# Performance work log

Hardware: AMD Instinct MI355X
Metric: run time of the kernel (lower is better)

The kernel has to match this reference:

```python
import jax, jax.numpy as jnp
import numpy as np

N = 50000      # entities
R = 400        # relations
D = 300        # init/hidden/output dim (hard-coded 300 in module)
E = 800000     # edges over N+R nodes
B = 2048       # aligned train pairs
L = 32         # padded neighbor sequence length
H, DK = 8, 32  # n_head=8, d_k=d_v=32
GAMMA1, GAMMA2 = 0.9, 0.2


def setup_inputs() -> dict:
    key = jax.random.key(0)
    ks = iter(jax.random.split(key, 48))
    nk = lambda: next(ks)
    inp = {}
    inp["e_x"] = jax.random.normal(nk(), (N, D), jnp.float32)
    inp["r_x"] = jax.random.normal(nk(), (R, 2 * D), jnp.float32)
    inp["edge_w"] = jax.random.uniform(nk(), (E,), jnp.float32)
    # learned params (fan-in scaled)
    s = lambda fi: 1.0 / np.sqrt(fi)
    inp["Wrel"] = jax.random.normal(nk(), (2 * D, D), jnp.float32) * s(2 * D)
    inp["brel"] = jnp.zeros((D,), jnp.float32)
    inp["W1"] = jax.random.normal(nk(), (D, D), jnp.float32) * s(D)
    inp["b1"] = jnp.zeros((D,), jnp.float32)
    inp["W2"] = jax.random.normal(nk(), (D, D), jnp.float32) * s(D)
    inp["b2"] = jnp.zeros((D,), jnp.float32)
    inp["Wprox"] = jax.random.normal(nk(), (2 * D, D), jnp.float32) * s(2 * D)
    inp["bprox"] = jnp.zeros((D,), jnp.float32)
    # encoder params, index 0 = input_encoder, 1 = output_encoder
    inp["enc_Wq"] = jax.random.normal(nk(), (2, D, H * DK), jnp.float32) * s(D)
    inp["enc_Wk"] = jax.random.normal(nk(), (2, D, H * DK), jnp.float32) * s(D)
    inp["enc_Wv"] = jax.random.normal(nk(), (2, D, H * DK), jnp.float32) * s(D)
    inp["enc_Wo"] = jax.random.normal(nk(), (2, H * DK, D), jnp.float32) * s(H * DK)
    # graph structure
    inp["edge_src"] = jax.random.randint(nk(), (E,), 0, N + R, jnp.int32)
    inp["edge_dst"] = jax.random.randint(nk(), (E,), 0, N + R, jnp.int32)
    # aligned entity pairs + padded neighbor (relation, head) sequences
    inp["l_ids"] = jax.random.randint(nk(), (B,), 0, N, jnp.int32)
    inp["r_ids"] = jax.random.randint(nk(), (B,), 0, N, jnp.int32)
    for p in ("l_in", "l_out", "r_in", "r_out"):
        inp[p + "_rel"] = jax.random.randint(nk(), (B, L), 0, R, jnp.int32)
        inp[p + "_head"] = jax.random.randint(nk(), (B, L), 0, N, jnp.int32)
        inp[p + "_mask"] = jax.random.randint(nk(), (B, L), 0, 2, jnp.int32).astype(bool)
    inp["train_len"] = B
    return inp


def _cosine(x, y):
    xn = x / jnp.maximum(jnp.linalg.norm(x, axis=1, keepdims=True), 1e-8)
    yn = y / jnp.maximum(jnp.linalg.norm(y, axis=1, keepdims=True), 1e-8)
    return xn @ yn.T


def _encoder(rel_seq, head_seq, mask, kernel, ent_f, rel_f, Wq, Wk, Wv, Wo):
    # neighbor tokens: relation emb + head entity emb    [B, L, D]
    tok = ent_f[head_seq] + rel_f[rel_seq]
    b = tok.shape[0]
    q = (kernel @ Wq).reshape(b, H, DK)                  # kernel entity is the query
    k = (tok @ Wk).reshape(b, L, H, DK)
    v = (tok @ Wv).reshape(b, L, H, DK)
    scores = jnp.einsum('bhd,blhd->bhl', q, k) / np.sqrt(DK)
    scores = jnp.where(mask[:, None, :], scores, -1e9)
    attn = jax.nn.softmax(scores, axis=-1)
    ctx = jnp.einsum('bhl,blhd->bhd', attn, v).reshape(b, H * DK)
    out = ctx @ Wo                                       # [B, D]
    # entities with empty neighbor list -> zero vector (original code path)
    return jnp.where(mask.any(-1)[:, None], out, 0.0)


def _get_proximity(ids, in_rel, in_head, in_mask, out_rel, out_head, out_mask,
                   ent_f, rel_f, enc_Wq, enc_Wk, enc_Wv, enc_Wo, Wprox, bprox):
    kernel = ent_f[ids]                                  # [B, D]
    in_em = _encoder(in_rel, in_head, in_mask, kernel, ent_f, rel_f,
                     enc_Wq[0], enc_Wk[0], enc_Wv[0], enc_Wo[0])
    out_em = _encoder(out_rel, out_head, out_mask, kernel, ent_f, rel_f,
                      enc_Wq[1], enc_Wk[1], enc_Wv[1], enc_Wo[1])
    prox = jnp.concatenate([in_em, out_em], axis=1) @ Wprox + bprox
    return jnp.concatenate([kernel, prox], axis=1)       # [B, 2D]


def reference(e_x, r_x, edge_w, Wrel, brel, W1, b1, W2, b2, Wprox, bprox,
              enc_Wq, enc_Wk, enc_Wv, enc_Wo,
              edge_src, edge_dst, l_ids, r_ids,
              l_in_rel, l_in_head, l_in_mask, l_out_rel, l_out_head, l_out_mask,
              r_in_rel, r_in_head, r_in_mask, r_out_rel, r_out_head, r_out_mask,
              train_len):
    NT = N + R
    # relation_linear then relational GCN over joint entity+relation graph
    r0 = r_x @ Wrel + brel                               # [R, D]
    x = jnp.concatenate([e_x, r0], axis=0)               # [NT, D]
    agg1 = jax.ops.segment_sum(edge_w[:, None] * x[edge_src], edge_dst, num_segments=NT)
    h1 = jax.nn.relu(agg1 @ W1 + b1)
    agg2 = jax.ops.segment_sum(edge_w[:, None] * h1[edge_src], edge_dst, num_segments=NT)
    h2 = agg2 @ W2 + b2
    gcn_ex, gcn_rx = h2[:N], h2[N:]
    # proximity embeddings for left/right aligned entities
    lem = _get_proximity(l_ids, l_in_rel, l_in_head, l_in_mask,
                         l_out_rel, l_out_head, l_out_mask,
                         gcn_ex, gcn_rx, enc_Wq, enc_Wk, enc_Wv, enc_Wo, Wprox, bprox)
    rem = _get_proximity(r_ids, r_in_rel, r_in_head, r_in_mask,
                         r_out_rel, r_out_head, r_out_mask,
                         gcn_ex, gcn_rx, enc_Wq, enc_Wk, enc_Wv, enc_Wo, Wprox, bprox)
    # contrastive alignment loss
    sim = _cosine(lem, rem)                              # [B, B]
    diag = jnp.diagonal(sim)
    pos_part = jnp.mean(jnp.minimum(diag, GAMMA1))
    no_diag = sim - jnp.diag(diag)
    neg_part = jnp.mean(jnp.maximum(no_diag, GAMMA2))
    loss = neg_part - GAMMA2 - pos_part + GAMMA1
    return loss, lem, rem
```

## Files before the change

### kernel.cpp

```cpp
#include <hip/hip_runtime.h>
#include <cstdint>
#include <cstddef>

typedef _Float16 f16;
typedef __attribute__((ext_vector_type(8))) _Float16 half8;
typedef __attribute__((ext_vector_type(4))) _Float16 half4;
typedef __attribute__((ext_vector_type(4))) float f32x4;

#define NE 50000
#define NR 400
#define DD 300
#define NTOT 50400
#define EE 800000
#define BB 2048
#define LL 32
#define HD 256
#define KP1 320
#define KP2 608

__device__ inline void split2h(float x, f16& hi, f16& lo) {
  f16 h = (f16)x;
  hi = h;
  lo = (f16)(x - (float)h);
}

__global__ void convert_f16_kernel(const float4* __restrict__ src, half4* __restrict__ dst,
                                   int n4) {
  int i = blockIdx.x * blockDim.x + threadIdx.x;
  if (i < n4) {
    float4 v = src[i];
    dst[i] = (half4){(f16)v.x, (f16)v.y, (f16)v.z, (f16)v.w};
  }
}

__global__ void rel_proj_kernel(const float* __restrict__ r_x, const float* __restrict__ Wrel,
                                const float* __restrict__ brel, f16* __restrict__ out) {
  int row = blockIdx.x;
  int c = threadIdx.x;
  if (c >= DD) return;
  float acc = brel[c];
  const float* rr = r_x + (size_t)row * (2 * DD);
  for (int k = 0; k < 2 * DD; ++k) acc += rr[k] * Wrel[(size_t)k * DD + c];
  out[(size_t)row * DD + c] = (f16)acc;
}

__global__ void hist_kernel(const int* __restrict__ dst, int* __restrict__ counts) {
  int e = blockIdx.x * blockDim.x + threadIdx.x;
  if (e < EE) atomicAdd(&counts[dst[e]], 1);
}

__global__ __launch_bounds__(1024) void scan_kernel(const int* __restrict__ counts,
                                                    int* __restrict__ row_ptr,
                                                    int* __restrict__ cursor) {
  __shared__ int sums[1024];
  const int n = NTOT;
  int t = threadIdx.x;
  const int chunk = (n + 1023) / 1024;
  int begin = t * chunk;
  int end = begin + chunk; if (end > n) end = n;
  int s = 0;
  for (int i = begin; i < end; ++i) s += counts[i];
  sums[t] = s;
  __syncthreads();
  for (int off = 1; off < 1024; off <<= 1) {
    int v = (t >= off) ? sums[t - off] : 0;
    __syncthreads();
    sums[t] += v;
    __syncthreads();
  }
  int run = sums[t] - s;
  for (int i = begin; i < end; ++i) {
    row_ptr[i] = run; cursor[i] = run;
    run += counts[i];
  }
  if (t == 1023) row_ptr[n] = sums[1023];
}

__global__ void scatter_kernel(const int* __restrict__ dst, const int* __restrict__ src,
                               const float* __restrict__ w, int* __restrict__ cursor,
                               int* __restrict__ src_s, float* __restrict__ w_s) {
  int e = blockIdx.x * blockDim.x + threadIdx.x;
  if (e < EE) {
    int pos = atomicAdd(&cursor[dst[e]], 1);
    src_s[pos] = src[e];
    w_s[pos] = w[e];
  }
}

__global__ void detect_mask_kernel(const unsigned* __restrict__ m0, const unsigned* __restrict__ m1,
                                   const unsigned* __restrict__ m2, const unsigned* __restrict__ m3,
                                   int* __restrict__ flag) {
  int idx = blockIdx.x * blockDim.x + threadIdx.x;
  const int wp = BB * LL / 4;
  if (idx >= 4 * wp) return;
  const unsigned* p = idx < wp ? m0 : idx < 2 * wp ? m1 : idx < 3 * wp ? m2 : m3;
  if (p[idx % wp] > 1u) atomicOr(flag, 1);
}

__global__ void norm_mask4_kernel(const void* __restrict__ r0, const void* __restrict__ r1,
                                  const void* __restrict__ r2, const void* __restrict__ r3,
                                  int* __restrict__ outm, int* __restrict__ many,
                                  const int* __restrict__ flag) {
  int idx = blockIdx.x * blockDim.x + threadIdx.x;
  if (idx >= 4 * BB * LL) return;
  int mi = idx / (BB * LL), k = idx % (BB * LL);
  const void* raw = mi == 0 ? r0 : mi == 1 ? r1 : mi == 2 ? r2 : r3;
  int v = (*flag) ? (int)((const unsigned char*)raw)[k] : ((const int*)raw)[k];
  v = v ? 1 : 0;
  outm[idx] = v;
  if (v) atomicOr(&many[idx >> 5], 1);
}

__global__ void concat_ids_kernel(const int* __restrict__ a, const int* __restrict__ b,
                                  int* __restrict__ o) {
  int i = blockIdx.x * blockDim.x + threadIdx.x;
  if (i < BB) o[i] = a[i];
  else if (i < 2 * BB) o[i] = b[i - BB];
}

__global__ __launch_bounds__(320) void aggregate_kernel(
    const f16* __restrict__ feat, f16* __restrict__ outhi, f16* __restrict__ outlo,
    const int* __restrict__ row_ptr, const int* __restrict__ srcs, const float* __restrict__ ws) {
  int d = blockIdx.x;
  int f = threadIdx.x;
  if (f >= DD) return;
  int beg = row_ptr[d], end = row_ptr[d + 1];
  float acc = 0.f;
  int e = beg;
  for (; e + 8 <= end; e += 8) {
    int s[8]; float wv[8]; float v[8];
#pragma unroll
    for (int u = 0; u < 8; ++u) { s[u] = srcs[e + u]; wv[u] = ws[e + u]; }
#pragma unroll
    for (int u = 0; u < 8; ++u) v[u] = (float)feat[(size_t)s[u] * DD + f];
#pragma unroll
    for (int u = 0; u < 8; ++u) acc += wv[u] * v[u];
  }
  for (; e + 2 <= end; e += 2) {
    int s0 = srcs[e], s1 = srcs[e + 1];
    float w0 = ws[e], w1 = ws[e + 1];
    acc += w0 * (float)feat[(size_t)s0 * DD + f] + w1 * (float)feat[(size_t)s1 * DD + f];
  }
  if (e < end) acc += ws[e] * (float)feat[(size_t)srcs[e] * DD + f];
  f16 hi, lo; split2h(acc, hi, lo);
  outhi[(size_t)d * KP1 + f] = hi;
  outlo[(size_t)d * KP1 + f] = lo;
}

__global__ void pad_zero_kernel(f16* __restrict__ hi, f16* __restrict__ lo, int rows, int ld, int c0) {
  int pw = ld - c0;
  int idx = blockIdx.x * blockDim.x + threadIdx.x;
  if (idx >= rows * pw) return;
  int r = idx / pw, c = c0 + idx % pw;
  hi[(size_t)r * ld + c] = (f16)0.f;
  if (lo) lo[(size_t)r * ld + c] = (f16)0.f;
}

#define N_TD 11
struct TDesc {
  const float* in; f16* oh; f16* ol;
  int Kreal, Nn, Kpad, tiles_x, tile_base;
};
struct TPack { TDesc d[N_TD]; };

__global__ __launch_bounds__(256) void transpose_multi_kernel(TPack p) {
  __shared__ float tile[32][33];
  int t = blockIdx.x;
  int e = 0;
#pragma unroll
  for (int i = 1; i < N_TD; ++i)
    if (t >= p.d[i].tile_base) e = i;
  TDesc dd = p.d[e];
  int local = t - dd.tile_base;
  int k0 = (local % dd.tiles_x) * 32, n0 = (local / dd.tiles_x) * 32;
  int tx = threadIdx.x & 31, ty = threadIdx.x >> 5;
#pragma unroll
  for (int r = 0; r < 4; ++r) {
    int k = k0 + ty + r * 8, n = n0 + tx;
    float v = (k < dd.Kreal && n < dd.Nn) ? dd.in[(size_t)k * dd.Nn + n] : 0.f;
    tile[ty + r * 8][tx] = v;
  }
  __syncthreads();
#pragma unroll
  for (int r = 0; r < 4; ++r) {
    int n = n0 + ty + r * 8, k = k0 + tx;
    if (n < dd.Nn && k < dd.Kpad) {
      f16 h, l; split2h(tile[tx][ty + r * 8], h, l);
      dd.oh[(size_t)n * dd.Kpad + k] = h;
      dd.ol[(size_t)n * dd.Kpad + k] = l;
    }
  }
}

__global__ __launch_bounds__(256, 2) void mfma_gemm_kernel(
    const f16* __restrict__ Ahi, const f16* __restrict__ Alo, int lda,
    const f16* __restrict__ Bhi, const f16* __restrict__ Blo, int ldb,
    int M, int Nn, int K, const int* __restrict__ g1,
    float* __restrict__ C, int ldc, int coloff,
    const float* __restrict__ bias, int dorelu, const int* __restrict__ rowmask,
    f16* __restrict__ Chi, f16* __restrict__ Clo, int ldc16,
    int npass, int wofuse, int losfuse, double* __restrict__ accum) {
  __shared__ int4 sAh[512], sAl[512], sBh[512], sBl[512];
  const int tid = threadIdx.x;
  const int row0 = blockIdx.y * 128, col0 = blockIdx.x * 128;
  const int wave = tid >> 6, lane = tid & 63;
  const int wrow = (wave >> 1) * 64, wcol = (wave & 1) * 64;
  const int m16 = lane & 15, quad = lane >> 4;

  const int sr = tid >> 2, sc = tid & 3;
  const f16* pah[2]; const f16* pal[2]; bool va[2];
  const f16* pbh[2]; const f16* pbl[2]; bool vb[2];
  int sidx[2];
#pragma unroll
  for (int i = 0; i < 2; ++i) {
    int r = sr + i * 64;
    sidx[i] = r * 4 + (sc ^ ((r >> 1) & 3));
    int grow = row0 + r;
    va[i] = grow < M;
    int ar = va[i] ? (g1 ? g1[grow] : grow) : 0;
    pah[i] = Ahi + (size_t)ar * lda + sc * 8;
    pal[i] = Alo + (size_t)ar * lda + sc * 8;
    int gn = col0 + r;
    vb[i] = gn < Nn;
    int br = vb[i] ? gn : 0;
    pbh[i] = Bhi + (size_t)br * ldb + sc * 8;
    pbl[i] = Blo + (size_t)br * ldb + sc * 8;
  }
  int idxA[4], idxB[4];
#pragma unroll
  for (int f = 0; f < 4; ++f) {
    int r = wrow + f * 16 + m16;
    idxA[f] = r * 4 + (quad ^ ((r >> 1) & 3));
    int n = wcol + f * 16 + m16;
    idxB[f] = n * 4 + (quad ^ ((n >> 1) & 3));
  }
  f32x4 acc[4][4];
#pragma unroll
  for (int i = 0; i < 4; ++i)
#pragma unroll
    for (int j = 0; j < 4; ++j) acc[i][j] = (f32x4){0.f, 0.f, 0.f, 0.f};

  const int4 z4 = {0, 0, 0, 0};
  for (int k0 = 0; k0 < K; k0 += 32) {
#pragma unroll
    for (int i = 0; i < 2; ++i) {
      int4 vh = z4, wh = z4;
      if (va[i]) vh = *(const int4*)(pah[i] + k0);
      if (vb[i]) wh = *(const int4*)(pbh[i] + k0);
      sAh[sidx[i]] = vh; sBh[sidx[i]] = wh;
      if (npass >= 2) {
        int4 vl = z4;
        if (va[i]) vl = *(const int4*)(pal[i] + k0);
        sAl[sidx[i]] = vl;
      }
      if (npass >= 3) {
        int4 wl = z4;
        if (vb[i]) wl = *(const int4*)(pbl[i] + k0);
        sBl[sidx[i]] = wl;
      }
    }
    __syncthreads();
    half8 ah[4], bh[4];
#pragma unroll
    for (int f = 0; f < 4; ++f) {
      ah[f] = *(const half8*)&sAh[idxA[f]];
      bh[f] = *(const half8*)&sBh[idxB[f]];
    }
#pragma unroll
    for (int i = 0; i < 4; ++i)
#pragma unroll
      for (int j = 0; j < 4; ++j)
        acc[i][j] = __builtin_amdgcn_mfma_f32_16x16x32_f16(ah[i], bh[j], acc[i][j], 0, 0, 0);
    if (npass >= 2) {
      half8 al[4];
#pragma unroll
      for (int f = 0; f < 4; ++f) al[f] = *(const half8*)&sAl[idxA[f]];
#pragma unroll
      for (int i = 0; i < 4; ++i)
#pragma unroll
        for (int j = 0; j < 4; ++j)
          acc[i][j] = __builtin_amdgcn_mfma_f32_16x16x32_f16(al[i], bh[j], acc[i][j], 0, 0, 0);
    }
    if (npass >= 3) {
      half8 bl[4];
#pragma unroll
      for (int f = 0; f < 4; ++f) bl[f] = *(const half8*)&sBl[idxB[f]];
#pragma unroll
      for (int i = 0; i < 4; ++i)
#pragma unroll
        for (int j = 0; j < 4; ++j)
          acc[i][j] = __builtin_amdgcn_mfma_f32_16x16x32_f16(ah[i], bl[j], acc[i][j], 0, 0, 0);
    }
    __syncthreads();
  }

  if (losfuse) {
    float negs = 0.f, poss = 0.f;
#pragma unroll
    for (int i = 0; i < 4; ++i)
#pragma unroll
      for (int reg = 0; reg < 4; ++reg) {
        int row = row0 + wrow + i * 16 + quad * 4 + reg;
#pragma unroll
        for (int j = 0; j < 4; ++j) {
          int col = col0 + wcol + j * 16 + m16;
          float s = acc[i][j][reg];
          if (row == col) { negs += 0.2f; poss += fminf(s, 0.9f); }
          else negs += fmaxf(s, 0.2f);
        }
      }
    float* rn_ = (float*)sAh;
    float* rp_ = (float*)sAl;
    rn_[tid] = negs; rp_[tid] = poss;
    __syncthreads();
    for (int off2 = 128; off2; off2 >>= 1) {
      if (tid < off2) { rn_[tid] += rn_[tid + off2]; rp_[tid] += rp_[tid + off2]; }
      __syncthreads();
    }
    if (tid == 0) {
      atomicAdd(&accum[0], (double)rn_[0]);
      atomicAdd(&accum[1], (double)rp_[0]);
    }
    return;
  }

#pragma unroll
  for (int i = 0; i < 4; ++i) {
#pragma unroll
    for (int reg = 0; reg < 4; ++reg) {
      int row = row0 + wrow + i * 16 + quad * 4 + reg;
      if (row >= M) continue;
      if (wofuse) {
        int b = row & 2047, side = (row >> 11) & 1, dir = (row >> 12) & 1;
        bool zero = rowmask[(side * 2 + dir) * BB + b] == 0;
        int orow = side * 2048 + b;
#pragma unroll
        for (int j = 0; j < 4; ++j) {
          int col = col0 + wcol + j * 16 + m16;
          if (col >= Nn) continue;
          if ((col >= 300) != (dir != 0)) continue;
          float v = acc[i][j][reg];
          if (zero) v = 0.f;
          f16 hb, lb; split2h(v, hb, lb);
          Chi[(size_t)orow * ldc16 + col] = hb;
          Clo[(size_t)orow * ldc16 + col] = lb;
        }
        continue;
      }
      bool zero = (rowmask != nullptr) && (rowmask[row] == 0);
#pragma unroll
      for (int j = 0; j < 4; ++j) {
        int col = col0 + wcol + j * 16 + m16;
        if (col >= Nn) continue;
        float v = acc[i][j][reg];
        if (bias) v += bias[col];
        if (dorelu) v = fmaxf(v, 0.f);
        if (zero) v = 0.f;
        if (C) C[(size_t)row * ldc + coloff + col] = v;
        if (Chi) {
          f16 hb, lb; split2h(v, hb, lb);
          Chi[(size_t)row * ldc16 + coloff + col] = hb;
          if (Clo) Clo[(size_t)row * ldc16 + coloff + col] = lb;
        }
      }
    }
  }
}

__global__ __launch_bounds__(256) void attention_kernel(
    const float* __restrict__ qAll, const f16* __restrict__ kv,
    const int* __restrict__ h00, const int* __restrict__ r00,
    const int* __restrict__ h01, const int* __restrict__ r01,
    const int* __restrict__ h10, const int* __restrict__ r10,
    const int* __restrict__ h11, const int* __restrict__ r11,
    const int* __restrict__ mask_norm, f16* __restrict__ ctxhi, f16* __restrict__ ctxlo) {
  int b = blockIdx.x;
  int y = blockIdx.y;
  int dir = y >> 1, side = y & 1;
  int tid = threadIdx.x;
  const int* hs = side ? (dir ? h11 : h10) : (dir ? h01 : h00);
  const int* rs = side ? (dir ? r11 : r10) : (dir ? r01 : r00);
  const int* msk = mask_norm + (size_t)(side * 2 + dir) * BB * LL;
  __shared__ float qs[256];
  __shared__ float attns[8][33];
  __shared__ int hid[32], rid[32], ms[32];
  qs[tid] = qAll[((size_t)(side * BB + b)) * 512 + dir * 256 + tid];
  if (tid < 32) {
    hid[tid] = hs[b * LL + tid];
    rid[tid] = NE + rs[b * LL + tid];
    ms[tid] = msk[b * LL + tid];
  }
  __syncthreads();
  int h = tid >> 5, l = tid & 31;
  const half8* k1 = (const half8*)(kv + (size_t)hid[l] * 1024 + dir * 512 + h * 32);
  const half8* k2 = (const half8*)(kv + (size_t)rid[l] * 1024 + dir * 512 + h * 32);
  float s = 0.f;
#pragma unroll
  for (int i = 0; i < 4; ++i) {
    half8 a = k1[i], c8 = k2[i];
    const float* qp = &qs[h * 32 + i * 8];
#pragma unroll
    for (int j = 0; j < 8; ++j) s += qp[j] * ((float)a[j] + (float)c8[j]);
  }
  s *= 0.17677669529663687f;
  s = ms[l] ? s : -1e9f;
  float m = s;
  for (int off = 16; off; off >>= 1) m = fmaxf(m, __shfl_xor(m, off, 32));
  float e = expf(s - m);
  float sum = e;
  for (int off = 16; off; off >>= 1) sum += __shfl_xor(sum, off, 32);
  attns[h][l] = e / sum;
  __syncthreads();
  int d = tid & 31;
  float c = 0.f;
#pragma unroll 4
  for (int l2 = 0; l2 < 32; ++l2) {
    float a = attns[h][l2];
    float v = (float)kv[(size_t)hid[l2] * 1024 + dir * 512 + 256 + h * 32 + d] +
              (float)kv[(size_t)rid[l2] * 1024 + dir * 512 + 256 + h * 32 + d];
    c += a * v;
  }
  f16 hb, lb; split2h(c, hb, lb);
  size_t o = ((size_t)(dir * 2 + side) * BB + b) * 256 + tid;
  ctxhi[o] = hb;
  ctxlo[o] = lb;
}

__global__ void gather_part_kernel(const f16* __restrict__ enthi, const f16* __restrict__ entlo,
                                   const int* __restrict__ ids, float* __restrict__ out) {
  int b = blockIdx.x;
  int t = threadIdx.x;
  if (t < DD) {
    size_t o = (size_t)ids[b] * KP1 + t;
    out[(size_t)b * 600 + t] = (float)enthi[o] + (float)entlo[o];
  }
}

__global__ __launch_bounds__(256) void rownorm_kernel(const float* __restrict__ rows,
                                                      f16* __restrict__ outhi,
                                                      f16* __restrict__ outlo) {
  int b = blockIdx.x;
  int t = threadIdx.x;
  const float* rp = rows + (size_t)b * 600;
  float s = 0.f;
  for (int c = t; c < 600; c += 256) { float v = rp[c]; s += v * v; }
  __shared__ float red[256];
  red[t] = s;
  __syncthreads();
  for (int off = 128; off; off >>= 1) {
    if (t < off) red[t] += red[t + off];
    __syncthreads();
  }
  __shared__ float inv;
  if (t == 0) inv = 1.f / fmaxf(sqrtf(red[0]), 1e-8f);
  __syncthreads();
  for (int c = t; c < KP2; c += 256) {
    float v = (c < 600) ? rp[c] * inv : 0.f;
    f16 hb, lb; split2h(v, hb, lb);
    outhi[(size_t)b * KP2 + c] = hb;
    outlo[(size_t)b * KP2 + c] = lb;
  }
}

__global__ void finalize_kernel(const double* __restrict__ accum, float* __restrict__ out) {
  double neg = accum[0] / ((double)BB * (double)BB);
  double pos = accum[1] / (double)BB;
  out[0] = (float)(neg - 0.2 - pos + 0.9);
}

static inline void launch_mfma(hipStream_t st, const f16* Ahi, const f16* Alo, int lda,
                               const f16* Bhi, const f16* Blo, int ldb, int M, int Nn, int K,
                               const int* g1, float* C, int ldc, int coloff, const float* bias,
                               int dorelu, const int* rowmask, f16* Chi, f16* Clo, int ldc16,
                               int npass = 3, int wofuse = 0, int losfuse = 0,
                               double* accum = nullptr) {
  dim3 grid((Nn + 127) / 128, (M + 127) / 128);
  mfma_gemm_kernel<<<grid, 256, 0, st>>>(Ahi, Alo, lda, Bhi, Blo, ldb, M, Nn, K, g1, C, ldc,
                                         coloff, bias, dorelu, rowmask, Chi, Clo, ldc16, npass,
                                         wofuse, losfuse, accum);
}

extern "C" void kernel_launch(void* const* d_in, const int* in_sizes, int n_in,
                              void* d_out, int out_size, void* d_ws, size_t ws_size,
                              hipStream_t stream) {
  const float* e_x    = (const float*)d_in[0];
  const float* r_x    = (const float*)d_in[1];
  const float* edge_w = (const float*)d_in[2];
  const float* Wrel   = (const float*)d_in[3];
  const float* brel   = (const float*)d_in[4];
  const float* W1     = (const float*)d_in[5];
  const float* b1     = (const float*)d_in[6];
  const float* W2     = (const float*)d_in[7];
  const float* b2     = (const float*)d_in[8];
  const float* Wprox  = (const float*)d_in[9];
  const float* bprox  = (const float*)d_in[10];
  const float* Wq     = (const float*)d_in[11];
  const float* Wk     = (const float*)d_in[12];
  const float* Wv     = (const float*)d_in[13];
  const float* Wo     = (const float*)d_in[14];
  const int* edge_src = (const int*)d_in[15];
  const int* edge_dst = (const int*)d_in[16];
  const int* l_ids    = (const int*)d_in[17];
  const int* r_ids    = (const int*)d_in[18];
  float* out = (float*)d_out;

  char* base = (char*)d_ws;
  size_t off = 0;
  auto nxt = [&](size_t bytes) -> char* {
    char* p = base + off;
    off += (bytes + 63) & ~(size_t)63;
    return p;
  };
  char* R0 = nxt(64512000);
  char* R1 = nxt(64512000);
  char* R2 = nxt(60480000);
  float* qAll  = (float*)nxt(8388608);
  f16* ctxAhi = (f16*)nxt(4194304);
  f16* ctxAlo = (f16*)nxt(4194304);
  f16* emAhi  = (f16*)nxt(4980736);
  f16* emAlo  = (f16*)nxt(4980736);
  f16* lnhi   = (f16*)nxt(2490368);
  f16* lnlo   = (f16*)nxt(2490368);
  f16* rnhi   = (f16*)nxt(2490368);
  f16* rnlo   = (f16*)nxt(2490368);
  f16* qkvhi  = (f16*)nxt(983040);
  f16* qkvlo  = (f16*)nxt(983040);
  f16* w12hi  = (f16*)nxt(384000);
  f16* w12lo  = (f16*)nxt(384000);
  f16* wohi   = (f16*)nxt(307200);
  f16* wolo   = (f16*)nxt(307200);
  f16* wpxhi  = (f16*)nxt(364800);
  f16* wpxlo  = (f16*)nxt(364800);
  double* accum = (double*)nxt(16);
  int* row_ptr  = (int*)nxt(4 * (NTOT + 1));
  int* cursor   = (int*)nxt(4 * NTOT);
  int* counts   = (int*)nxt(4 * NTOT);
  int* src_s    = (int*)nxt(4 * EE);
  float* w_s    = (float*)nxt(4 * EE);
  int* mask_norm = (int*)nxt(4 * 4 * BB * LL);
  int* maskany   = (int*)nxt(4 * 4 * BB);
  int* idsAll    = (int*)nxt(4 * 2 * BB);
  int* flag      = (int*)nxt(64);

  f16* xbuf16 = (f16*)R0;
  f16* h2hi = (f16*)R0;  f16* h2lo = h2hi + (size_t)NTOT * KP1;
  f16* agghi = (f16*)R1; f16* agglo = agghi + (size_t)NTOT * KP1;
  f16* kvAll = (f16*)R1;
  f16* h1f16 = (f16*)R2;

  hipMemsetAsync(counts, 0, NTOT * sizeof(int), stream);
  hipMemsetAsync(maskany, 0, 4 * BB * sizeof(int), stream);
  hipMemsetAsync(flag, 0, sizeof(int), stream);
  hipMemsetAsync(accum, 0, 2 * sizeof(double), stream);

  convert_f16_kernel<<<(3750000 + 255) / 256, 256, 0, stream>>>((const float4*)e_x,
                                                                (half4*)xbuf16, 3750000);
  rel_proj_kernel<<<NR, 320, 0, stream>>>(r_x, Wrel, brel, xbuf16 + (size_t)NE * DD);

  hist_kernel<<<(EE + 255) / 256, 256, 0, stream>>>(edge_dst, counts);
  scan_kernel<<<1, 1024, 0, stream>>>(counts, row_ptr, cursor);
  scatter_kernel<<<(EE + 255) / 256, 256, 0, stream>>>(edge_dst, edge_src, edge_w, cursor, src_s,
                                                       w_s);

  detect_mask_kernel<<<256, 256, 0, stream>>>((const unsigned*)d_in[21], (const unsigned*)d_in[24],
                                              (const unsigned*)d_in[27], (const unsigned*)d_in[30],
                                              flag);
  norm_mask4_kernel<<<(4 * BB * LL + 255) / 256, 256, 0, stream>>>(
      d_in[21], d_in[24], d_in[27], d_in[30], mask_norm, maskany, flag);
  concat_ids_kernel<<<(2 * BB + 255) / 256, 256, 0, stream>>>(l_ids, r_ids, idsAll);

  {
    TPack p;
    int tb = 0, idx = 0;
    auto add = [&](const float* in, f16* oh, f16* ol, int Kreal, int Nn, int Kpad) {
      int txs = (Kpad + 31) / 32, tys = (Nn + 31) / 32;
      p.d[idx] = TDesc{in, oh, ol, Kreal, Nn, Kpad, txs, tb};
      tb += txs * tys;
      ++idx;
    };
    add(Wq,             qkvhi + 0 * 81920, qkvlo + 0 * 81920, 300, 256, KP1);
    add(Wq + 300 * 256, qkvhi + 1 * 81920, qkvlo + 1 * 81920, 300, 256, KP1);
    add(Wk,             qkvhi + 2 * 81920, qkvlo + 2 * 81920, 300, 256, KP1);
    add(Wv,             qkvhi + 3 * 81920, qkvlo + 3 * 81920, 300, 256, KP1);
    add(Wk + 300 * 256, qkvhi + 4 * 81920, qkvlo + 4 * 81920, 300, 256, KP1);
    add(Wv + 300 * 256, qkvhi + 5 * 81920, qkvlo + 5 * 81920, 300, 256, KP1);
    add(W1,             w12hi,             w12lo,             300, 300, KP1);
    add(W2,             w12hi + 96000,     w12lo + 96000,     300, 300, KP1);
    add(Wo,             wohi,              wolo,              256, 300, 256);
    add(Wo + 256 * 300, wohi + 76800,      wolo + 76800,      256, 300, 256);
    add(Wprox,          wpxhi,             wpxlo,             600, 300, KP2);
    transpose_multi_kernel<<<tb, 256, 0, stream>>>(p);
  }

  pad_zero_kernel<<<(NTOT * 20 + 255) / 256, 256, 0, stream>>>(agghi, agglo, NTOT, KP1, 300);
  pad_zero_kernel<<<(4096 * 8 + 255) / 256, 256, 0, stream>>>(emAhi, emAlo, 4096, KP2, 600);

  aggregate_kernel<<<NTOT, 320, 0, stream>>>(xbuf16, agghi, agglo, row_ptr, src_s, w_s);
  launch_mfma(stream, agghi, agglo, KP1, w12hi, w12lo, KP1, NTOT, 300, KP1, nullptr, nullptr, 0,
              0, b1, 1, nullptr, h1f16, nullptr, 300, 2);
  aggregate_kernel<<<NTOT, 320, 0, stream>>>(h1f16, agghi, agglo, row_ptr, src_s, w_s);
  pad_zero_kernel<<<(NTOT * 20 + 255) / 256, 256, 0, stream>>>(h2hi, h2lo, NTOT, KP1, 300);
  launch_mfma(stream, agghi, agglo, KP1, w12hi + 96000, w12lo + 96000, KP1, NTOT, 300, KP1,
              nullptr, nullptr, 0, 0, b2, 0, nullptr, h2hi, h2lo, KP1, 3);

  launch_mfma(stream, h2hi, h2lo, KP1, qkvhi, qkvlo, KP1, 2 * BB, 512, KP1, idsAll, qAll, 512, 0,
              nullptr, 0, nullptr, nullptr, nullptr, 0, 2);

  launch_mfma(stream, h2hi, h2lo, KP1, qkvhi + 2 * 81920, qkvlo + 2 * 81920, KP1, NTOT, 1024,
              KP1, nullptr, nullptr, 0, 0, nullptr, 0, nullptr, kvAll, nullptr, 1024, 2);

  attention_kernel<<<dim3(BB, 4), 256, 0, stream>>>(
      qAll, kvAll,
      (const int*)d_in[20], (const int*)d_in[19],
      (const int*)d_in[23], (const int*)d_in[22],
      (const int*)d_in[26], (const int*)d_in[25],
      (const int*)d_in[29], (const int*)d_in[28],
      mask_norm, ctxAhi, ctxAlo);

  launch_mfma(stream, ctxAhi, ctxAlo, 256, wohi, wolo, 256, 4 * BB, 600, 256, nullptr, nullptr,
              0, 0, nullptr, 0, maskany, emAhi, emAlo, KP2, 3, 1);

  float* lem = out + 1;
  float* rem = out + 1 + (size_t)BB * 600;
  launch_mfma(stream, emAhi, emAlo, KP2, wpxhi, wpxlo, KP2, 4096, 300, KP2, nullptr, lem, 600,
              300, bprox, 0, nullptr, nullptr, nullptr, 0, 3);
  gather_part_kernel<<<BB, 320, 0, stream>>>(h2hi, h2lo, l_ids, lem);
  gather_part_kernel<<<BB, 320, 0, stream>>>(h2hi, h2lo, r_ids, rem);

  rownorm_kernel<<<BB, 256, 0, stream>>>(lem, lnhi, lnlo);
  rownorm_kernel<<<BB, 256, 0, stream>>>(rem, rnhi, rnlo);
  launch_mfma(stream, lnhi, lnlo, KP2, rnhi, rnlo, KP2, BB, BB, KP2, nullptr, nullptr, 0, 0,
              nullptr, 0, nullptr, nullptr, nullptr, 0, 1, 0, 1, accum);
  finalize_kernel<<<1, 1, 0, stream>>>(accum, out);
}
```

Measured before the change: 1.174 ms.

## Template GEMM on pass count and N-tiles, fuse padding, gathers and rownorms

Templates the split-fp16 MFMA GEMM on pass count and a wider 256-column tile, so large-N GEMMs reuse each A tile across two B tiles and dead pass branches are compiled out. Zero-padding moves into the aggregate kernel and the GEMM epilogues, which removes the pad_zero launches. The entity-embedding gather moves into the proximity GEMM epilogue, and the left and right rownorm launches merge into one. This cuts launch count and redundant A-tile loads, at the cost of higher register and LDS use in the NT=2 variant, which may lower occupancy.

Result: slower. 1.277 ms (+8.8%).

```diff
diff --git a/kernel.cpp b/kernel.cpp
--- a/kernel.cpp
+++ b/kernel.cpp
@@ -123,7 +123,11 @@
     const int* __restrict__ row_ptr, const int* __restrict__ srcs, const float* __restrict__ ws) {
   int d = blockIdx.x;
   int f = threadIdx.x;
-  if (f >= DD) return;
+  if (f >= DD) {
+    outhi[(size_t)d * KP1 + f] = (f16)0.f;
+    outlo[(size_t)d * KP1 + f] = (f16)0.f;
+    return;
+  }
   int beg = row_ptr[d], end = row_ptr[d + 1];
   float acc = 0.f;
   int e = beg;
@@ -145,15 +149,6 @@
   f16 hi, lo; split2h(acc, hi, lo);
   outhi[(size_t)d * KP1 + f] = hi;
   outlo[(size_t)d * KP1 + f] = lo;
-}
-
-__global__ void pad_zero_kernel(f16* __restrict__ hi, f16* __restrict__ lo, int rows, int ld, int c0) {
-  int pw = ld - c0;
-  int idx = blockIdx.x * blockDim.x + threadIdx.x;
-  if (idx >= rows * pw) return;
-  int r = idx / pw, c = c0 + idx % pw;
-  hi[(size_t)r * ld + c] = (f16)0.f;
-  if (lo) lo[(size_t)r * ld + c] = (f16)0.f;
 }
 
 #define N_TD 11
@@ -192,34 +187,44 @@
   }
 }
 
+template <int NPASS, int NT>
 __global__ __launch_bounds__(256, 2) void mfma_gemm_kernel(
     const f16* __restrict__ Ahi, const f16* __restrict__ Alo, int lda,
     const f16* __restrict__ Bhi, const f16* __restrict__ Blo, int ldb,
-    int M, int Nn, int K, const int* __restrict__ g1,
+    int M, int Nn, int padTo, int K, const int* __restrict__ g1,
     float* __restrict__ C, int ldc, int coloff,
     const float* __restrict__ bias, int dorelu, const int* __restrict__ rowmask,
     f16* __restrict__ Chi, f16* __restrict__ Clo, int ldc16,
-    int npass, int wofuse, int losfuse, double* __restrict__ accum) {
-  __shared__ int4 sAh[512], sAl[512], sBh[512], sBl[512];
+    int wofuse, int losfuse, double* __restrict__ accum,
+    const f16* __restrict__ g2hi, const f16* __restrict__ g2lo, const int* __restrict__ gids) {
+  constexpr int BR = 128 * NT;
+  __shared__ int4 sAh[512];
+  __shared__ int4 sAl[(NPASS >= 2) ? 512 : 1];
+  __shared__ int4 sBh[BR * 4];
+  __shared__ int4 sBl[(NPASS >= 3) ? BR * 4 : 1];
   const int tid = threadIdx.x;
-  const int row0 = blockIdx.y * 128, col0 = blockIdx.x * 128;
+  const int row0 = blockIdx.y * 128, col0 = blockIdx.x * BR;
   const int wave = tid >> 6, lane = tid & 63;
   const int wrow = (wave >> 1) * 64, wcol = (wave & 1) * 64;
   const int m16 = lane & 15, quad = lane >> 4;
 
   const int sr = tid >> 2, sc = tid & 3;
-  const f16* pah[2]; const f16* pal[2]; bool va[2];
-  const f16* pbh[2]; const f16* pbl[2]; bool vb[2];
-  int sidx[2];
+  const f16* pah[2]; const f16* pal[2]; bool va[2]; int sidxA[2];
 #pragma unroll
   for (int i = 0; i < 2; ++i) {
     int r = sr + i * 64;
-    sidx[i] = r * 4 + (sc ^ ((r >> 1) & 3));
+    sidxA[i] = r * 4 + (sc ^ ((r >> 1) & 3));
     int grow = row0 + r;
     va[i] = grow < M;
     int ar = va[i] ? (g1 ? g1[grow] : grow) : 0;
     pah[i] = Ahi + (size_t)ar * lda + sc * 8;
     pal[i] = Alo + (size_t)ar * lda + sc * 8;
+  }
+  const f16* pbh[2 * NT]; const f16* pbl[2 * NT]; bool vb[2 * NT]; int sidxB[2 * NT];
+#pragma unroll
+  for (int i = 0; i < 2 * NT; ++i) {
+    int r = sr + i * 64;
+    sidxB[i] = r * 4 + (sc ^ ((r >> 1) & 3));
     int gn = col0 + r;
     vb[i] = gn < Nn;
     int br = vb[i] ? gn : 0;
@@ -234,62 +239,75 @@
     int n = wcol + f * 16 + m16;
     idxB[f] = n * 4 + (quad ^ ((n >> 1) & 3));
   }
-  f32x4 acc[4][4];
-#pragma unroll
-  for (int i = 0; i < 4; ++i)
-#pragma unroll
-    for (int j = 0; j < 4; ++j) acc[i][j] = (f32x4){0.f, 0.f, 0.f, 0.f};
+  f32x4 acc[NT][4][4];
+#pragma unroll
+  for (int nt = 0; nt < NT; ++nt)
+#pragma unroll
+    for (int i = 0; i < 4; ++i)
+#pragma unroll
+      for (int j = 0; j < 4; ++j) acc[nt][i][j] = (f32x4){0.f, 0.f, 0.f, 0.f};
 
   const int4 z4 = {0, 0, 0, 0};
   for (int k0 = 0; k0 < K; k0 += 32) {
 #pragma unroll
     for (int i = 0; i < 2; ++i) {
-      int4 vh = z4, wh = z4;
+      int4 vh = z4;
       if (va[i]) vh = *(const int4*)(pah[i] + k0);
-      if (vb[i]) wh = *(const int4*)(pbh[i] + k0);
-      sAh[sidx[i]] = vh; sBh[sidx[i]] = wh;
-      if (npass >= 2) {
+      sAh[sidxA[i]] = vh;
+      if constexpr (NPASS >= 2) {
         int4 vl = z4;
         if (va[i]) vl = *(const int4*)(pal[i] + k0);
-        sAl[sidx[i]] = vl;
+        sAl[sidxA[i]] = vl;
       }
-      if (npass >= 3) {
+    }
+#pragma unroll
+    for (int i = 0; i < 2 * NT; ++i) {
+      int4 wh = z4;
+      if (vb[i]) wh = *(const int4*)(pbh[i] + k0);
+      sBh[sidxB[i]] = wh;
+      if constexpr (NPASS >= 3) {
         int4 wl = z4;
         if (vb[i]) wl = *(const int4*)(pbl[i] + k0);
-        sBl[sidx[i]] = wl;
+        sBl[sidxB[i]] = wl;
       }
     }
     __syncthreads();
-    half8 ah[4], bh[4];
-#pragma unroll
-    for (int f = 0; f < 4; ++f) {
-      ah[f] = *(const half8*)&sAh[idxA[f]];
-      bh[f] = *(const half8*)&sBh[idxB[f]];
-    }
-#pragma unroll
-    for (int i = 0; i < 4; ++i)
-#pragma unroll
-      for (int j = 0; j < 4; ++j)
-        acc[i][j] = __builtin_amdgcn_mfma_f32_16x16x32_f16(ah[i], bh[j], acc[i][j], 0, 0, 0);
-    if (npass >= 2) {
-      half8 al[4];
-#pragma unroll
-      for (int f = 0; f < 4; ++f) al[f] = *(const half8*)&sAl[idxA[f]];
+    half8 ah[4];
+#pragma unroll
+    for (int f = 0; f < 4; ++f) ah[f] = *(const half8*)&sAh[idxA[f]];
+#pragma unroll
+    for (int nt = 0; nt < NT; ++nt) {
+      half8 bh[4];
+#pragma unroll
+      for (int f = 0; f < 4; ++f) bh[f] = *(const half8*)&sBh[idxB[f] + nt * 512];
 #pragma unroll
       for (int i = 0; i < 4; ++i)
 #pragma unroll
         for (int j = 0; j < 4; ++j)
-          acc[i][j] = __builtin_amdgcn_mfma_f32_16x16x32_f16(al[i], bh[j], acc[i][j], 0, 0, 0);
-    }
-    if (npass >= 3) {
-      half8 bl[4];
-#pragma unroll
-      for (int f = 0; f < 4; ++f) bl[f] = *(const half8*)&sBl[idxB[f]];
-#pragma unroll
-      for (int i = 0; i < 4; ++i)
-#pragma unroll
-        for (int j = 0; j < 4; ++j)
-          acc[i][j] = __builtin_amdgcn_mfma_f32_16x16x32_f16(ah[i], bl[j], acc[i][j], 0, 0, 0);
+          acc[nt][i][j] = __builtin_amdgcn_mfma_f32_16x16x32_f16(ah[i], bh[j], acc[nt][i][j],
+                                                                 0, 0, 0);
+      if constexpr (NPASS >= 2) {
+        half8 al[4];
+#pragma unroll
+        for (int f = 0; f < 4; ++f) al[f] = *(const half8*)&sAl[idxA[f]];
+#pragma unroll
+        for (int i = 0; i < 4; ++i)
+#pragma unroll
+          for (int j = 0; j < 4; ++j)
+            acc[nt][i][j] = __builtin_amdgcn_mfma_f32_16x16x32_f16(al[i], bh[j], acc[nt][i][j],
+                                                                   0, 0, 0);
+      }
+      if constexpr (NPASS >= 3) {
+        half8 bl[4];
+#pragma unroll
+        for (int f = 0; f < 4; ++f) bl[f] = *(const half8*)&sBl[idxB[f] + nt * 512];
+#pragma unroll
+        for (int i = 0; i < 4; ++i)
+#pragma unroll
+          for (int j = 0; j < 4; ++j)
+            acc[nt][i][j] = __builtin_amdgcn_mfma_f32_16x16x32_f16(ah[i], bl[j], acc[nt][i][j],
+                                                                   0, 0, 0);
+      }
     }
     __syncthreads();
   }
@@ -304,13 +322,13 @@
 #pragma unroll
         for (int j = 0; j < 4; ++j) {
           int col = col0 + wcol + j * 16 + m16;
-          float s = acc[i][j][reg];
+          float s = acc[0][i][j][reg];
           if (row == col) { negs += 0.2f; poss += fminf(s, 0.9f); }
           else negs += fmaxf(s, 0.2f);
         }
       }
     float* rn_ = (float*)sAh;
-    float* rp_ = (float*)sAl;
+    float* rp_ = rn_ + 256;
     rn_[tid] = negs; rp_[tid] = poss;
     __syncthreads();
     for (int off2 = 128; off2; off2 >>= 1) {
@@ -325,42 +343,57 @@
   }
 
 #pragma unroll
-  for (int i = 0; i < 4; ++i) {
-#pragma unroll
-    for (int reg = 0; reg < 4; ++reg) {
-      int row = row0 + wrow + i * 16 + quad * 4 + reg;
-      if (row >= M) continue;
-      if (wofuse) {
-        int b = row & 2047, side = (row >> 11) & 1, dir = (row >> 12) & 1;
-        bool zero = rowmask[(side * 2 + dir) * BB + b] == 0;
-        int orow = side * 2048 + b;
+  for (int nt = 0; nt < NT; ++nt) {
+#pragma unroll
+    for (int i = 0; i < 4; ++i) {
+#pragma unroll
+      for (int reg = 0; reg < 4; ++reg) {
+        int row = row0 + wrow + i * 16 + quad * 4 + reg;
+        if (row >= M) continue;
+        if (wofuse) {
+          int b = row & 2047, side = (row >> 11) & 1, dir = (row >> 12) & 1;
+          bool zero = rowmask[(side * 2 + dir) * BB + b] == 0;
+          int orow = side * 2048 + b;
+#pragma unroll
+          for (int j = 0; j < 4; ++j) {
+            int col = col0 + nt * 128 + wcol + j * 16 + m16;
+            if (col >= padTo) continue;
+            if (col >= Nn) {
+              Chi[(size_t)orow * ldc16 + col] = (f16)0.f;
+              Clo[(size_t)orow * ldc16 + col] = (f16)0.f;
+              continue;
+            }
+            if ((col >= 300) != (dir != 0)) continue;
+            float v = acc[nt][i][j][reg];
+            if (zero) v = 0.f;
+            f16 hb, lb; split2h(v, hb, lb);
+            Chi[(size_t)orow * ldc16 + col] = hb;
+            Clo[(size_t)orow * ldc16 + col] = lb;
+          }
+          continue;
+        }
+        bool zero = (rowmask != nullptr) && (rowmask[row] == 0);
 #pragma unroll
         for (int j = 0; j < 4; ++j) {
-          int col = col0 + wcol + j * 16 + m16;
-          if (col >= Nn) continue;
-          if ((col >= 300) != (dir != 0)) continue;
-          float v = acc[i][j][reg];
-          if (zero) v = 0.f;
-          f16 hb, lb; split2h(v, hb, lb);
-          Chi[(size_t)orow * ldc16 + col] = hb;
-          Clo[(size_t)orow * ldc16 + col] = lb;
-        }
-        continue;
-      }
-      bool zero = (rowmask != nullptr) && (rowmask[row] == 0);
-#pragma unroll
-      for (int j = 0; j < 4; ++j) {
-        int col = col0 + wcol + j * 16 + m16;
-        if (col >= Nn) continue;
-        float v = acc[i][j][reg];
-        if (bias) v += bias[col];
-        if (dorelu) v = fmaxf(v, 0.f);
-        if (zero) v = 0.f;
-        if (C) C[(size_t)row * ldc + coloff + col] = v;
-        if (Chi) {
-          f16 hb, lb; split2h(v, hb, lb);
-          Chi[(size_t)row * ldc16 + coloff + col] = hb;
-          if (Clo) Clo[(size_t)row * ldc16 + coloff + col] = lb;
+          int col = col0 + nt * 128 + wcol + j * 16 + m16;
+          if (col >= padTo) continue;
+          float v = 0.f;
+          if (col < Nn) {
+            v = acc[nt][i][j][reg];
+            if (bias) v += bias[col];
+            if (dorelu) v = fmaxf(v, 0.f);
+            if (zero) v = 0.f;
+          }
+          if (C) C[(size_t)row * ldc + coloff + col] = v;
+          if (Chi) {
+            f16 hb, lb; split2h(v, hb, lb);
+            Chi[(size_t)row * ldc16 + coloff + col] = hb;
+            if (Clo) Clo[(size_t)row * ldc16 + coloff + col] = lb;
+          }
+          if (gids && col < Nn) {
+            size_t go = (size_t)gids[row] * KP1 + col;
+            C[(size_t)row * ldc + col] = (float)g2hi[go] + (float)g2lo[go];
+          }
         }
       }
     }
@@ -426,16 +459,6 @@
   ctxlo[o] = lb;
 }
 
-__global__ void gather_part_kernel(const f16* __restrict__ enthi, const f16* __restrict__ entlo,
-                                   const int* __restrict__ ids, float* __restrict__ out) {
-  int b = blockIdx.x;
-  int t = threadIdx.x;
-  if (t < DD) {
-    size_t o = (size_t)ids[b] * KP1 + t;
-    out[(size_t)b * 600 + t] = (float)enthi[o] + (float)entlo[o];
-  }
-}
-
 __global__ __launch_bounds__(256) void rownorm_kernel(const float* __restrict__ rows,
                                                       f16* __restrict__ outhi,
                                                       f16* __restrict__ outlo) {
@@ -468,16 +491,29 @@
   out[0] = (float)(neg - 0.2 - pos + 0.9);
 }
 
-static inline void launch_mfma(hipStream_t st, const f16* Ahi, const f16* Alo, int lda,
-                               const f16* Bhi, const f16* Blo, int ldb, int M, int Nn, int K,
-                               const int* g1, float* C, int ldc, int coloff, const float* bias,
-                               int dorelu, const int* rowmask, f16* Chi, f16* Clo, int ldc16,
-                               int npass = 3, int wofuse = 0, int losfuse = 0,
-                               double* accum = nullptr) {
-  dim3 grid((Nn + 127) / 128, (M + 127) / 128);
-  mfma_gemm_kernel<<<grid, 256, 0, st>>>(Ahi, Alo, lda, Bhi, Blo, ldb, M, Nn, K, g1, C, ldc,
-                                         coloff, bias, dorelu, rowmask, Chi, Clo, ldc16, npass,
-                                         wofuse, losfuse, accum);
+static inline void launch_mfma(hipStream_t st, int npass, int nt,
+                               const f16* Ahi, const f16* Alo, int lda,
+                               const f16* Bhi, const f16* Blo, int ldb, int M, int Nn, int padTo,
+                               int K, const int* g1, float* C, int ldc, int coloff,
+                               const float* bias, int dorelu, const int* rowmask,
+                               f16* Chi, f16* Clo, int ldc16,
+                               int wofuse = 0, int losfuse = 0, double* accum = nullptr,
+                               const f16* g2hi = nullptr, const f16* g2lo = nullptr,
+                               const int* gids = nullptr) {
+  int bw = 128 * nt;
+  dim3 grid((Nn + bw - 1) / bw, (M + 127) / 128);
+#define ARGS Ahi, Alo, lda, Bhi, Blo, ldb, M, Nn, padTo, K, g1, C, ldc, coloff, bias, dorelu, \
+             rowmask, Chi, Clo, ldc16, wofuse, losfuse, accum, g2hi, g2lo, gids
+  if (nt == 2) {
+    mfma_gemm_kernel<2, 2><<<grid, 256, 0, st>>>(ARGS);
+  } else if (npass == 1) {
+    mfma_gemm_kernel<1, 1><<<grid, 256, 0, st>>>(ARGS);
+  } else if (npass == 2) {
+    mfma_gemm_kernel<2, 1><<<grid, 256, 0, st>>>(ARGS);
+  } else {
+    mfma_gemm_kernel<3, 1><<<grid, 256, 0, st>>>(ARGS);
+  }
+#undef ARGS
 }
 
 extern "C" void kernel_launch(void* const* d_in, const int* in_sizes, int n_in,
@@ -519,10 +555,8 @@
   f16* ctxAlo = (f16*)nxt(4194304);
   f16* emAhi  = (f16*)nxt(4980736);
   f16* emAlo  = (f16*)nxt(4980736);
-  f16* lnhi   = (f16*)nxt(2490368);
-  f16* lnlo   = (f16*)nxt(2490368);
-  f16* rnhi   = (f16*)nxt(2490368);
-  f16* rnlo   = (f16*)nxt(2490368);
+  f16* lnAhi  = (f16*)nxt(4980736);
+  f16* lnAlo  = (f16*)nxt(4980736);
   f16* qkvhi  = (f16*)nxt(983040);
   f16* qkvlo  = (f16*)nxt(983040);
   f16* w12hi  = (f16*)nxt(384000);
@@ -592,22 +626,18 @@
     transpose_multi_kernel<<<tb, 256, 0, stream>>>(p);
   }
 
-  pad_zero_kernel<<<(NTOT * 20 + 255) / 256, 256, 0, stream>>>(agghi, agglo, NTOT, KP1, 300);
-  pad_zero_kernel<<<(4096 * 8 + 255) / 256, 256, 0, stream>>>(emAhi, emAlo, 4096, KP2, 600);
-
   aggregate_kernel<<<NTOT, 320, 0, stream>>>(xbuf16, agghi, agglo, row_ptr, src_s, w_s);
-  launch_mfma(stream, agghi, agglo, KP1, w12hi, w12lo, KP1, NTOT, 300, KP1, nullptr, nullptr, 0,
-              0, b1, 1, nullptr, h1f16, nullptr, 300, 2);
+  launch_mfma(stream, 2, 2, agghi, agglo, KP1, w12hi, w12lo, KP1, NTOT, 300, 300, KP1, nullptr,
+              nullptr, 0, 0, b1, 1, nullptr, h1f16, nullptr, 300);
   aggregate_kernel<<<NTOT, 320, 0, stream>>>(h1f16, agghi, agglo, row_ptr, src_s, w_s);
-  pad_zero_kernel<<<(NTOT * 20 + 255) / 256, 256, 0, stream>>>(h2hi, h2lo, NTOT, KP1, 300);
-  launch_mfma(stream, agghi, agglo, KP1, w12hi + 96000, w12lo + 96000, KP1, NTOT, 300, KP1,
-              nullptr, nullptr, 0, 0, b2, 0, nullptr, h2hi, h2lo, KP1, 3);
-
-  launch_mfma(stream, h2hi, h2lo, KP1, qkvhi, qkvlo, KP1, 2 * BB, 512, KP1, idsAll, qAll, 512, 0,
-              nullptr, 0, nullptr, nullptr, nullptr, 0, 2);
-
-  launch_mfma(stream, h2hi, h2lo, KP1, qkvhi + 2 * 81920, qkvlo + 2 * 81920, KP1, NTOT, 1024,
-              KP1, nullptr, nullptr, 0, 0, nullptr, 0, nullptr, kvAll, nullptr, 1024, 2);
+  launch_mfma(stream, 3, 1, agghi, agglo, KP1, w12hi + 96000, w12lo + 96000, KP1, NTOT, 300, KP1,
+              KP1, nullptr, nullptr, 0, 0, b2, 0, nullptr, h2hi, h2lo, KP1);
+
+  launch_mfma(stream, 2, 1, h2hi, h2lo, KP1, qkvhi, qkvlo, KP1, 2 * BB, 512, 512, KP1, idsAll,
+              qAll, 512, 0, nullptr, 0, nullptr, nullptr, nullptr, 0);
+
+  launch_mfma(stream, 2, 2, h2hi, h2lo, KP1, qkvhi + 2 * 81920, qkvlo + 2 * 81920, KP1, NTOT,
+              1024, 1024, KP1, nullptr, nullptr, 0, 0, nullptr, 0, nullptr, kvAll, nullptr, 1024);
 
   attention_kernel<<<dim3(BB, 4), 256, 0, stream>>>(
       qAll, kvAll,
@@ -617,19 +647,17 @@
       (const int*)d_in[29], (const int*)d_in[28],
       mask_norm, ctxAhi, ctxAlo);
 
-  launch_mfma(stream, ctxAhi, ctxAlo, 256, wohi, wolo, 256, 4 * BB, 600, 256, nullptr, nullptr,
-              0, 0, nullptr, 0, maskany, emAhi, emAlo, KP2, 3, 1);
+  launch_mfma(stream, 3, 1, ctxAhi, ctxAlo, 256, wohi, wolo, 256, 4 * BB, 600, KP2, 256, nullptr,
+              nullptr, 0, 0, nullptr, 0, maskany, emAhi, emAlo, KP2, 1);
 
   float* lem = out + 1;
-  float* rem = out + 1 + (size_t)BB * 600;
-  launch_mfma(stream, emAhi, emAlo, KP2, wpxhi, wpxlo, KP2, 4096, 300, KP2, nullptr, lem, 600,
-              300, bprox, 0, nullptr, nullptr, nullptr, 0, 3);
-  gather_part_kernel<<<BB, 320, 0, stream>>>(h2hi, h2lo, l_ids, lem);
-  gather_part_kernel<<<BB, 320, 0, stream>>>(h2hi, h2lo, r_ids, rem);
-
-  rownorm_kernel<<<BB, 256, 0, stream>>>(lem, lnhi, lnlo);
-  rownorm_kernel<<<BB, 256, 0, stream>>>(rem, rnhi, rnlo);
-  launch_mfma(stream, lnhi, lnlo, KP2, rnhi, rnlo, KP2, BB, BB, KP2, nullptr, nullptr, 0, 0,
-              nullptr, 0, nullptr, nullptr, nullptr, 0, 1, 0, 1, accum);
+  launch_mfma(stream, 3, 1, emAhi, emAlo, KP2, wpxhi, wpxlo, KP2, 4096, 300, 300, KP2, nullptr,
+              lem, 600, 300, bprox, 0, nullptr, nullptr, nullptr, 0, 0, 0, nullptr, h2hi, h2lo,
+              idsAll);
+
+  rownorm_kernel<<<2 * BB, 256, 0, stream>>>(lem, lnAhi, lnAlo);
+  launch_mfma(stream, 1, 1, lnAhi, lnAlo, KP2, lnAhi + (size_t)BB * KP2, lnAlo + (size_t)BB * KP2,
+              KP2, BB, BB, BB, KP2, nullptr, nullptr, 0, 0, nullptr, 0, nullptr, nullptr, nullptr,
+              0, 0, 1, accum);
   finalize_kernel<<<1, 1, 0, stream>>>(accum, out);
 }
```
